# Kernel tuning notes

Measured on AMD Instinct MI355X. Metric: run time of the kernel, lower is better.

Reference implementation:

```python
import jax, jax.numpy as jnp
import numpy as np

IMG_DIM = 512


def _grid_q(img_dim):
    # matches torch module: q = [repeat(x, D), tile(y, D)] -> shape [2, D*D]
    x = np.arange(img_dim)
    q = np.stack([np.repeat(x, img_dim), np.tile(x, img_dim)], axis=0)
    return jnp.asarray(q, jnp.float32)


def _get_pixel(point, neighbor, imflat, img_dim):
    # point, neighbor: [N,2,HW]; imflat: [N,3,HW]
    w = 1.0 - jnp.abs(point - neighbor)          # [N,2,HW]
    weight = w[:, 0] * w[:, 1]                   # [N,HW]
    inds = (neighbor[:, 1] + img_dim * neighbor[:, 0]).astype(jnp.int32)  # y + D*x, [N,HW]
    # fused gather over all 3 channels (original does 3 separate torch.gather)
    pix = jnp.take_along_axis(imflat, inds[:, None, :], axis=2)  # [N,3,HW]
    return weight[:, None, :] * pix


def _get_masked_rp(image, mask, qi_orig, img_dim):
    N, Cc, H, W = image.shape
    imflat = image.reshape(N, Cc, H * W)
    qi_rescale = qi_orig * img_dim
    qi = jnp.clip(qi_rescale, 0.001, img_dim - 1.001)
    xf = jnp.floor(qi[:, 0:1]); yf = jnp.floor(qi[:, 1:2])
    xc = jnp.ceil(qi[:, 0:1]);  yc = jnp.ceil(qi[:, 1:2])
    res = (_get_pixel(qi, jnp.concatenate([xf, yf], axis=1), imflat, img_dim)
         + _get_pixel(qi, jnp.concatenate([xc, yf], axis=1), imflat, img_dim)
         + _get_pixel(qi, jnp.concatenate([xf, yc], axis=1), imflat, img_dim)
         + _get_pixel(qi, jnp.concatenate([xc, yc], axis=1), imflat, img_dim))
    oob_loss = jnp.mean((qi_rescale - qi) ** 2) / (img_dim ** 2) * 0.0001
    res_img = res.reshape(image.shape)
    return res_img * mask, oob_loss  # mask broadcasts [N,1,H,W] -> [N,3,H,W]


def setup_inputs() -> dict:
    key = jax.random.key(0)
    k1, k2, k3, k4, k5 = jax.random.split(key, 5)
    N, D = 16, IMG_DIM
    im1 = jax.random.normal(k1, (N, 3, D, D), dtype=jnp.float32)
    im2 = jax.random.normal(k2, (N, 3, D, D), dtype=jnp.float32)
    C = jax.random.normal(k3, (N, 2, D, D), dtype=jnp.float32)
    M1 = jax.random.uniform(k4, (N, 1, D, D), dtype=jnp.float32)
    M2 = jax.random.uniform(k5, (N, 1, D, D), dtype=jnp.float32)
    return {"im1": im1, "im2": im2, "C": C, "M1": M1, "M2": M2}


def reference(im1, im2, C, M1, M2):
    img_dim = im1.shape[-1]
    N = C.shape[0]
    Cflat = C.reshape(N, 2, -1)                 # [N,2,HW]
    total_mask = M1 + M2
    M1n = M1 / total_mask
    M2n = M2 / total_mask
    q = _grid_q(img_dim)[None]                  # [1,2,HW], broadcasts to [N,2,HW]
    a, oob_a = _get_masked_rp(im1, M1n, q + Cflat, img_dim)
    b, oob_b = _get_masked_rp(im2, M2n, q - Cflat, img_dim)
    return a + b, oob_a + oob_b
```

## Files before the change

kernel.cpp:

```cpp
#include <hip/hip_runtime.h>

#define D     512
#define HW    (D * D)
#define BLOCK 256

__device__ __forceinline__ void samp_gather(const float* __restrict__ im,
    float rx, float ry, float m, float r3[3], float* oob)
{
    float cxq = fminf(fmaxf(rx, 0.001f), 510.999f);
    float cyq = fminf(fmaxf(ry, 0.001f), 510.999f);
    float dx = rx - cxq, dy = ry - cyq;
    *oob += dx * dx + dy * dy;
    float xff = floorf(cxq), xcf = ceilf(cxq);
    float yff = floorf(cyq), ycf = ceilf(cyq);
    float wxf = 1.0f - (cxq - xff), wxc = 1.0f - (xcf - cxq);
    float wyf = 1.0f - (cyq - yff), wyc = 1.0f - (ycf - cyq);
    float w00 = wxf * wyf, w10 = wxc * wyf, w01 = wxf * wyc, w11 = wxc * wyc;
    int xf = (int)xff, xc = (int)xcf, yf = (int)yff, yc = (int)ycf;
    int i00 = yf + D * xf, i10 = yf + D * xc;
    int i01 = yc + D * xf, i11 = yc + D * xc;
#pragma unroll
    for (int c = 0; c < 3; ++c) {
        const float* __restrict__ ch = im + (size_t)c * HW;
        r3[c] += m * (w00 * ch[i00] + w10 * ch[i10] + w01 * ch[i01] + w11 * ch[i11]);
    }
}

__global__ void __launch_bounds__(BLOCK) vm_kernel(
    const float* __restrict__ im1, const float* __restrict__ im2,
    const float* __restrict__ C,   const float* __restrict__ M1,
    const float* __restrict__ M2,  float* __restrict__ out,
    double* __restrict__ partials)
{
    int b = blockIdx.x;
    int n = b >> 9;
    int i = b & (D - 1);
    int j0 = threadIdx.x * 2;

    const float* base1 = im1 + (size_t)n * 3 * HW;
    const float* base2 = im2 + (size_t)n * 3 * HW;

    const float WF = 1.0f - (510.999f - 510.0f);
    const float WC = 1.0f - (511.0f - 510.999f);
    float S1[3], S2[3];
#pragma unroll
    for (int c = 0; c < 3; ++c) {
        const float* c1 = base1 + (size_t)c * HW;
        const float* c2 = base2 + (size_t)c * HW;
        S1[c] = (WF * WF) * c1[510 + D * 510] + (WC * WF) * c1[510 + D * 511]
              + (WF * WC) * c1[511 + D * 510] + (WC * WC) * c1[511 + D * 511];
        S2[c] = (WF * WF) * c2[510 + D * 510] + (WC * WF) * c2[510 + D * 511]
              + (WF * WC) * c2[511 + D * 510] + (WC * WC) * c2[511 + D * 511];
    }

    size_t cb = (size_t)n * 2 * HW, mb = (size_t)n * HW, ob = (size_t)n * 3 * HW;
    size_t pp = (size_t)i * D + j0;

    float2 cx2 = *(const float2*)(C  + cb + pp);
    float2 cy2 = *(const float2*)(C  + cb + HW + pp);
    float2 m12 = *(const float2*)(M1 + mb + pp);
    float2 m22 = *(const float2*)(M2 + mb + pp);

    float fi = (float)i;
    float o0[2], o1[2], o2[2];
    float oob = 0.0f;

#pragma unroll
    for (int k = 0; k < 2; ++k) {
        float cx  = k ? cx2.y : cx2.x;
        float cy  = k ? cy2.y : cy2.x;
        float m1v = k ? m12.y : m12.x;
        float m2v = k ? m22.y : m22.x;
        float fj  = (float)(j0 + k);

        float tot = m1v + m2v;
        float inv = 1.0f / tot;
        float m1n = m1v * inv, m2n = m2v * inv;

        float rx1 = (fi + cx) * 512.0f, ry1 = (fj + cy) * 512.0f;
        float rx2 = (fi - cx) * 512.0f, ry2 = (fj - cy) * 512.0f;

        bool fast = ((fi - fabsf(cx)) * 512.0f >= 510.999f)
                 && ((fj - fabsf(cy)) * 512.0f >= 510.999f);

        float r3[3];
        if (fast) {
            float dx1 = rx1 - 510.999f, dy1 = ry1 - 510.999f;
            float dx2 = rx2 - 510.999f, dy2 = ry2 - 510.999f;
            oob += dx1 * dx1 + dy1 * dy1 + dx2 * dx2 + dy2 * dy2;
            r3[0] = m1n * S1[0] + m2n * S2[0];
            r3[1] = m1n * S1[1] + m2n * S2[1];
            r3[2] = m1n * S1[2] + m2n * S2[2];
        } else {
            r3[0] = r3[1] = r3[2] = 0.0f;
            samp_gather(base1, rx1, ry1, m1n, r3, &oob);
            samp_gather(base2, rx2, ry2, m2n, r3, &oob);
        }
        o0[k] = r3[0]; o1[k] = r3[1]; o2[k] = r3[2];
    }

    *(float2*)(out + ob + pp)          = make_float2(o0[0], o0[1]);
    *(float2*)(out + ob + HW + pp)     = make_float2(o1[0], o1[1]);
    *(float2*)(out + ob + 2 * HW + pp) = make_float2(o2[0], o2[1]);

    for (int off = 32; off > 0; off >>= 1)
        oob += __shfl_down(oob, off, 64);

    __shared__ float soob[BLOCK / 64];
    int lane = threadIdx.x & 63;
    int w    = threadIdx.x >> 6;
    if (lane == 0) soob[w] = oob;
    __syncthreads();
    if (threadIdx.x == 0)
        partials[blockIdx.x] = (double)soob[0] + (double)soob[1]
                             + (double)soob[2] + (double)soob[3];
}

__global__ void __launch_bounds__(BLOCK) reduce_kernel(
    const double* __restrict__ partials, int nparts,
    float* __restrict__ out_last, double scale)
{
    double s = 0.0;
    for (int i = threadIdx.x; i < nparts; i += BLOCK)
        s += partials[i];
    for (int off = 32; off > 0; off >>= 1)
        s += __shfl_down(s, off, 64);

    __shared__ double sm[BLOCK / 64];
    int lane = threadIdx.x & 63;
    int w    = threadIdx.x >> 6;
    if (lane == 0) sm[w] = s;
    __syncthreads();
    if (threadIdx.x == 0)
        *out_last = (float)((sm[0] + sm[1] + sm[2] + sm[3]) * scale);
}

extern "C" void kernel_launch(void* const* d_in, const int* in_sizes, int n_in,
                              void* d_out, int out_size, void* d_ws, size_t ws_size,
                              hipStream_t stream) {
    const float* im1 = (const float*)d_in[0];
    const float* im2 = (const float*)d_in[1];
    const float* C   = (const float*)d_in[2];
    const float* M1  = (const float*)d_in[3];
    const float* M2  = (const float*)d_in[4];
    float* out = (float*)d_out;
    double* ws = (double*)d_ws;

    int N = in_sizes[3] / HW;
    int blocks = N * D;

    vm_kernel<<<blocks, BLOCK, 0, stream>>>(im1, im2, C, M1, M2, out, ws);

    double scale = 1.0 / ((double)N * 2.0 * (double)HW) / (double)HW * 1e-4;
    reduce_kernel<<<1, BLOCK, 0, stream>>>(ws, blocks, out + (out_size - 1), scale);
}
```

Measured before the change: 200.5 us.

## Process four rows per block and write per-wave partials without shared sync

```diff
diff --git a/kernel.cpp b/kernel.cpp
--- a/kernel.cpp
+++ b/kernel.cpp
@@ -3,6 +3,7 @@
 #define D     512
 #define HW    (D * D)
 #define BLOCK 256
+#define RPB   4
 
 __device__ __forceinline__ void samp_gather(const float* __restrict__ im,
     float rx, float ry, float m, float r3[3], float* oob)
@@ -32,10 +33,12 @@
     const float* __restrict__ M2,  float* __restrict__ out,
     double* __restrict__ partials)
 {
-    int b = blockIdx.x;
-    int n = b >> 9;
-    int i = b & (D - 1);
-    int j0 = threadIdx.x * 2;
+    int b  = blockIdx.x;
+    int n  = b >> 7;
+    int i0 = (b & 127) * RPB;
+    int w  = threadIdx.x >> 6;
+    int l  = threadIdx.x & 63;
+    int c0 = w * 128 + l * 2;
 
     const float* base1 = im1 + (size_t)n * 3 * HW;
     const float* base2 = im2 + (size_t)n * 3 * HW;
@@ -54,66 +57,69 @@
     }
 
     size_t cb = (size_t)n * 2 * HW, mb = (size_t)n * HW, ob = (size_t)n * 3 * HW;
-    size_t pp = (size_t)i * D + j0;
 
-    float2 cx2 = *(const float2*)(C  + cb + pp);
-    float2 cy2 = *(const float2*)(C  + cb + HW + pp);
-    float2 m12 = *(const float2*)(M1 + mb + pp);
-    float2 m22 = *(const float2*)(M2 + mb + pp);
+    float2 cxv[RPB], cyv[RPB], m1v[RPB], m2v[RPB];
+    size_t roff[RPB];
+#pragma unroll
+    for (int r = 0; r < RPB; ++r) {
+        roff[r] = (size_t)(i0 + r) * D + c0;
+        cxv[r] = *(const float2*)(C  + cb + roff[r]);
+        cyv[r] = *(const float2*)(C  + cb + HW + roff[r]);
+        m1v[r] = *(const float2*)(M1 + mb + roff[r]);
+        m2v[r] = *(const float2*)(M2 + mb + roff[r]);
+    }
 
-    float fi = (float)i;
-    float o0[2], o1[2], o2[2];
+    float o0[RPB][2], o1[RPB][2], o2[RPB][2];
     float oob = 0.0f;
+#pragma unroll
+    for (int r = 0; r < RPB; ++r) {
+        float fi = (float)(i0 + r);
+#pragma unroll
+        for (int k = 0; k < 2; ++k) {
+            float cx  = k ? cxv[r].y : cxv[r].x;
+            float cy  = k ? cyv[r].y : cyv[r].x;
+            float m1s = k ? m1v[r].y : m1v[r].x;
+            float m2s = k ? m2v[r].y : m2v[r].x;
+            float fj  = (float)(c0 + k);
+
+            float tot = m1s + m2s;
+            float inv = 1.0f / tot;
+            float m1n = m1s * inv, m2n = m2s * inv;
+
+            float rx1 = (fi + cx) * 512.0f, ry1 = (fj + cy) * 512.0f;
+            float rx2 = (fi - cx) * 512.0f, ry2 = (fj - cy) * 512.0f;
+
+            bool fast = ((fi - fabsf(cx)) * 512.0f >= 510.999f)
+                     && ((fj - fabsf(cy)) * 512.0f >= 510.999f);
+
+            float r3[3];
+            if (fast) {
+                float dx1 = rx1 - 510.999f, dy1 = ry1 - 510.999f;
+                float dx2 = rx2 - 510.999f, dy2 = ry2 - 510.999f;
+                oob += dx1 * dx1 + dy1 * dy1 + dx2 * dx2 + dy2 * dy2;
+                r3[0] = m1n * S1[0] + m2n * S2[0];
+                r3[1] = m1n * S1[1] + m2n * S2[1];
+                r3[2] = m1n * S1[2] + m2n * S2[2];
+            } else {
+                r3[0] = r3[1] = r3[2] = 0.0f;
+                samp_gather(base1, rx1, ry1, m1n, r3, &oob);
+                samp_gather(base2, rx2, ry2, m2n, r3, &oob);
+            }
+            o0[r][k] = r3[0]; o1[r][k] = r3[1]; o2[r][k] = r3[2];
+        }
+    }
 
 #pragma unroll
-    for (int k = 0; k < 2; ++k) {
-        float cx  = k ? cx2.y : cx2.x;
-        float cy  = k ? cy2.y : cy2.x;
-        float m1v = k ? m12.y : m12.x;
-        float m2v = k ? m22.y : m22.x;
-        float fj  = (float)(j0 + k);
-
-        float tot = m1v + m2v;
-        float inv = 1.0f / tot;
-        float m1n = m1v * inv, m2n = m2v * inv;
-
-        float rx1 = (fi + cx) * 512.0f, ry1 = (fj + cy) * 512.0f;
-        float rx2 = (fi - cx) * 512.0f, ry2 = (fj - cy) * 512.0f;
-
-        bool fast = ((fi - fabsf(cx)) * 512.0f >= 510.999f)
-                 && ((fj - fabsf(cy)) * 512.0f >= 510.999f);
-
-        float r3[3];
-        if (fast) {
-            float dx1 = rx1 - 510.999f, dy1 = ry1 - 510.999f;
-            float dx2 = rx2 - 510.999f, dy2 = ry2 - 510.999f;
-            oob += dx1 * dx1 + dy1 * dy1 + dx2 * dx2 + dy2 * dy2;
-            r3[0] = m1n * S1[0] + m2n * S2[0];
-            r3[1] = m1n * S1[1] + m2n * S2[1];
-            r3[2] = m1n * S1[2] + m2n * S2[2];
-        } else {
-            r3[0] = r3[1] = r3[2] = 0.0f;
-            samp_gather(base1, rx1, ry1, m1n, r3, &oob);
-            samp_gather(base2, rx2, ry2, m2n, r3, &oob);
-        }
-        o0[k] = r3[0]; o1[k] = r3[1]; o2[k] = r3[2];
+    for (int r = 0; r < RPB; ++r) {
+        *(float2*)(out + ob + roff[r])          = make_float2(o0[r][0], o0[r][1]);
+        *(float2*)(out + ob + HW + roff[r])     = make_float2(o1[r][0], o1[r][1]);
+        *(float2*)(out + ob + 2 * HW + roff[r]) = make_float2(o2[r][0], o2[r][1]);
     }
-
-    *(float2*)(out + ob + pp)          = make_float2(o0[0], o0[1]);
-    *(float2*)(out + ob + HW + pp)     = make_float2(o1[0], o1[1]);
-    *(float2*)(out + ob + 2 * HW + pp) = make_float2(o2[0], o2[1]);
 
     for (int off = 32; off > 0; off >>= 1)
         oob += __shfl_down(oob, off, 64);
-
-    __shared__ float soob[BLOCK / 64];
-    int lane = threadIdx.x & 63;
-    int w    = threadIdx.x >> 6;
-    if (lane == 0) soob[w] = oob;
-    __syncthreads();
-    if (threadIdx.x == 0)
-        partials[blockIdx.x] = (double)soob[0] + (double)soob[1]
-                             + (double)soob[2] + (double)soob[3];
+    if (l == 0)
+        partials[(size_t)b * (BLOCK / 64) + w] = (double)oob;
 }
 
 __global__ void __launch_bounds__(BLOCK) reduce_kernel(
@@ -147,10 +153,11 @@
     double* ws = (double*)d_ws;
 
     int N = in_sizes[3] / HW;
-    int blocks = N * D;
+    int blocks = N * (D / RPB);
+    int nparts = blocks * (BLOCK / 64);
 
     vm_kernel<<<blocks, BLOCK, 0, stream>>>(im1, im2, C, M1, M2, out, ws);
 
     double scale = 1.0 / ((double)N * 2.0 * (double)HW) / (double)HW * 1e-4;
-    reduce_kernel<<<1, BLOCK, 0, stream>>>(ws, blocks, out + (out_size - 1), scale);
+    reduce_kernel<<<1, BLOCK, 0, stream>>>(ws, nparts, out + (out_size - 1), scale);
 }
```

After: 228.6 us. 1.14x slower.
